# Optimization experiments

Measured on AMD Instinct MI355X. Metric: run time of the kernel, lower is better.

## Reference

```python
import jax, jax.numpy as jnp
import numpy as np

ALPHA = 1.0  # set_privacy(True)


def setup_inputs() -> dict:
    key = jax.random.key(0)
    k1, k2, k3, k4, k5, k6 = jax.random.split(key, 6)
    B, S, IN, OUT = 2, 1024, 4096, 11008
    NNZ = 2250000
    x = jax.random.normal(k1, (B, S, IN), dtype=jnp.float32)
    scales = jax.random.uniform(k2, (OUT,), dtype=jnp.float32)  # positive per-row scales
    ortho_vals = jax.random.normal(k3, (NNZ,), dtype=jnp.float32)
    base_packed = jax.random.randint(k4, (OUT, IN // 2), 0, 256, dtype=jnp.int32)
    ortho_rows = jnp.sort(jax.random.randint(k5, (NNZ,), 0, OUT, dtype=jnp.int32))
    ortho_cols = jax.random.randint(k6, (NNZ,), 0, IN, dtype=jnp.int32)
    return {"x": x, "scales": scales, "ortho_vals": ortho_vals,
            "base_packed": base_packed, "ortho_rows": ortho_rows, "ortho_cols": ortho_cols}


def _dequant_weight(base_packed, scales):
    OUT, HALF = base_packed.shape
    low = base_packed & 0xF          # packed column 2j  -> original column 2j
    high = (base_packed >> 4) & 0xF  # packed column 2j  -> original column 2j+1
    # interleave low/high nibbles back to [OUT, IN]
    w_off = jnp.stack([low, high], axis=-1).reshape(OUT, 2 * HALF)
    return (w_off.astype(jnp.float32) - 8.0) * scales[:, None]


def reference(x, scales, ortho_vals, base_packed, ortho_rows, ortho_cols):
    OUT = base_packed.shape[0]
    IN = base_packed.shape[1] * 2
    w_base = _dequant_weight(base_packed, scales)  # [OUT, IN] fp32
    w_sparse = jnp.zeros((OUT, IN), dtype=jnp.float32).at[ortho_rows, ortho_cols].add(
        ortho_vals.astype(jnp.float32))
    w = w_base + ALPHA * w_sparse
    x_flat = x.reshape(-1, IN).astype(jnp.float32)
    out = x_flat @ w.T  # [tokens, OUT]
    return out.reshape(x.shape[:-1] + (OUT,)).astype(x.dtype)
```

## Files before the change

### kernel.cpp

```cpp
#include <hip/hip_runtime.h>
#include <stdint.h>

#define ALPHA 1.0f

typedef int i32x4 __attribute__((ext_vector_type(4)));

typedef __attribute__((address_space(3))) void lds_void_t;
typedef const __attribute__((address_space(1))) void global_void_t;

__device__ __forceinline__ void async16(const void* g, void* l) {
    __builtin_amdgcn_global_load_lds((global_void_t*)g, (lds_void_t*)l, 16, 0, 0);
}

__device__ __forceinline__ signed char q8(float v, float inv) {
    float f = fminf(fmaxf(v * inv, -127.f), 127.f);
    return (signed char)__float2int_rn(f);
}

__global__ __launch_bounds__(256) void prep_kernel(
    const float* __restrict__ x, const int* __restrict__ rows,
    int* __restrict__ rstart, int* __restrict__ rend,
    signed char* __restrict__ X8, float* __restrict__ sx, int M, int nnz) {
    const int b = blockIdx.x;
    if (b < M) {
        __shared__ float red[4];
        const int t = threadIdx.x;
        const float4* xr = (const float4*)(x + (size_t)b * 4096);
        float4 v[4];
        float mx = 0.f;
#pragma unroll
        for (int i = 0; i < 4; i++) {
            v[i] = xr[t * 4 + i];
            mx = fmaxf(mx, fmaxf(fmaxf(fabsf(v[i].x), fabsf(v[i].y)),
                                 fmaxf(fabsf(v[i].z), fabsf(v[i].w))));
        }
#pragma unroll
        for (int o = 32; o > 0; o >>= 1) mx = fmaxf(mx, __shfl_xor(mx, o));
        if ((t & 63) == 0) red[t >> 6] = mx;
        __syncthreads();
        mx = fmaxf(fmaxf(red[0], red[1]), fmaxf(red[2], red[3]));
        mx = fmaxf(mx, 1e-20f);
        if (t == 0) sx[b] = mx / 127.f;
        const float inv = 127.f / mx;
        union { signed char c[16]; int4 w; } u;
#pragma unroll
        for (int i = 0; i < 4; i++) {
            u.c[i * 4 + 0] = q8(v[i].x, inv);
            u.c[i * 4 + 1] = q8(v[i].y, inv);
            u.c[i * 4 + 2] = q8(v[i].z, inv);
            u.c[i * 4 + 3] = q8(v[i].w, inv);
        }
        ((int4*)(X8 + (size_t)b * 4096))[t] = u.w;
    } else {
        int i = (b - M) * 256 + threadIdx.x;
        if (i < nnz) {
            int r = rows[i];
            if (i == 0 || rows[i - 1] != r) rstart[r] = i;
            if (i == nnz - 1 || rows[i + 1] != r) rend[r] = i + 1;
        }
    }
}

__global__ __launch_bounds__(256) void build_w8_kernel(
    const int* __restrict__ packed, const float* __restrict__ scales,
    const float* __restrict__ vals, const int* __restrict__ cols,
    const int* __restrict__ rstart, const int* __restrict__ rend,
    signed char* __restrict__ W8, float* __restrict__ sw) {
    __shared__ __align__(16) float acc[4096];
    __shared__ float red[4];
    const int r = blockIdx.x;
    const int t = threadIdx.x;
    const float s = scales[r];

    const int4* prow4 = (const int4*)(packed + (size_t)r * 2048);
    int4 p0 = prow4[2 * t], p1 = prow4[2 * t + 1];

    const int lo = rstart[r], hi = rend[r];

    float4 sp[4] = {float4{0,0,0,0}, float4{0,0,0,0},
                    float4{0,0,0,0}, float4{0,0,0,0}};
    if (hi > lo) {
        char* ab = (char*)acc;
#pragma unroll
        for (int i = 0; i < 4; i++) {
            int b = 64 * t + 16 * i;
            *(float4*)(ab + (b ^ (((b >> 7) & 7) << 4))) = float4{0, 0, 0, 0};
        }
        __syncthreads();
        for (int i = lo + t; i < hi; i += 256) {
            int b = cols[i] * 4;
            atomicAdd((float*)(ab + (b ^ (((b >> 7) & 7) << 4))),
                      vals[i] * ALPHA);
        }
        __syncthreads();
#pragma unroll
        for (int i = 0; i < 4; i++) {
            int b = 64 * t + 16 * i;
            sp[i] = *(const float4*)(ab + (b ^ (((b >> 7) & 7) << 4)));
        }
    }

    float w[16];
    {
        int pv[8] = {p0.x, p0.y, p0.z, p0.w, p1.x, p1.y, p1.z, p1.w};
#pragma unroll
        for (int q = 0; q < 8; q++) {
            w[2 * q]     = (float)((pv[q] & 0xF) - 8) * s;
            w[2 * q + 1] = (float)(((pv[q] >> 4) & 0xF) - 8) * s;
        }
    }
    const float* spf = (const float*)sp;
    float mx = 0.f;
#pragma unroll
    for (int k = 0; k < 16; k++) {
        w[k] += spf[k];
        mx = fmaxf(mx, fabsf(w[k]));
    }
#pragma unroll
    for (int o = 32; o > 0; o >>= 1) mx = fmaxf(mx, __shfl_xor(mx, o));
    if ((t & 63) == 0) red[t >> 6] = mx;
    __syncthreads();
    mx = fmaxf(fmaxf(red[0], red[1]), fmaxf(red[2], red[3]));
    mx = fmaxf(mx, 1e-20f);
    if (t == 0) sw[r] = mx / 127.f;
    const float inv = 127.f / mx;

    union { signed char c[16]; int4 v; } u;
#pragma unroll
    for (int k = 0; k < 16; k++) u.c[k] = q8(w[k], inv);
    ((int4*)(W8 + (size_t)r * 4096))[t] = u.v;
}

__global__ __launch_bounds__(512) void gemm_kernel(
    const signed char* __restrict__ Xq,
    const signed char* __restrict__ Wq,
    const float* __restrict__ sx,
    const float* __restrict__ sw,
    float* __restrict__ C,
    int M, int N, int K) {
    __shared__ __align__(16) signed char smem[3 * 49152];

    const int tid  = threadIdx.x;
    const int wid  = tid >> 6;
    const int lane = tid & 63;
    const int wr = wid >> 2;
    const int wc = wid & 3;

    const int nwg = gridDim.x;
    const int bid = blockIdx.x;
    const int qc = nwg >> 3, rr = nwg & 7;
    const int xcd = bid & 7, loc = bid >> 3;
    const int swz = (xcd < rr ? xcd * (qc + 1) : rr * (qc + 1) + (xcd - rr) * qc) + loc;
    const int tm = M >> 7;
    const int mt = swz % tm;
    const int nt = swz / tm;
    const int m0 = mt << 7;
    const int n0 = nt << 8;

    const int sr = tid >> 3;
    const int sc = ((tid & 7) ^ (sr & 7)) << 4;
    const int lw0 = wid << 10;
    const int lw1 = 8192 + (wid << 10);

    const signed char* Ax  = Xq + (size_t)m0 * K;
    const signed char* Bw0 = Wq + (size_t)n0 * K;
    const signed char* Bw1 = Wq + (size_t)(n0 + 128) * K;

#define STAGE(gbase, ldsbase) do {                                         \
        async16((gbase) + (size_t)sr * K + sc, (ldsbase) + lw0);           \
        async16((gbase) + (size_t)(sr + 64) * K + sc, (ldsbase) + lw1);    \
    } while (0)

    const int fm = lane & 15;
    const int slot0 = ((lane >> 4) ^ (lane & 7)) << 4;
    const int slot1 = slot0 ^ 64;
    const int arow_base = wr * 64;
    const int brow_base = wc * 64;

#define LDA(buf, mi, sl) \
    (*(const i32x4*)((buf) + (size_t)(arow_base + (mi) * 16 + fm) * 128 + (sl)))
#define LDB(buf, nj, sl) \
    (*(const i32x4*)((buf) + 16384 + (size_t)(brow_base + (nj) * 16 + fm) * 128 + (sl)))

#define MFMA8(m0i, m1i, aX, aY, B0, B1, B2, B3) do {                        \
        __builtin_amdgcn_s_setprio(1);                                      \
        acc[m0i][0] = __builtin_amdgcn_mfma_i32_16x16x64_i8(aX, B0, acc[m0i][0], 0, 0, 0); \
        acc[m1i][0] = __builtin_amdgcn_mfma_i32_16x16x64_i8(aY, B0, acc[m1i][0], 0, 0, 0); \
        acc[m0i][1] = __builtin_amdgcn_mfma_i32_16x16x64_i8(aX, B1, acc[m0i][1], 0, 0, 0); \
        acc[m1i][1] = __builtin_amdgcn_mfma_i32_16x16x64_i8(aY, B1, acc[m1i][1], 0, 0, 0); \
        acc[m0i][2] = __builtin_amdgcn_mfma_i32_16x16x64_i8(aX, B2, acc[m0i][2], 0, 0, 0); \
        acc[m1i][2] = __builtin_amdgcn_mfma_i32_16x16x64_i8(aY, B2, acc[m1i][2], 0, 0, 0); \
        acc[m0i][3] = __builtin_amdgcn_mfma_i32_16x16x64_i8(aX, B3, acc[m0i][3], 0, 0, 0); \
        acc[m1i][3] = __builtin_amdgcn_mfma_i32_16x16x64_i8(aY, B3, acc[m1i][3], 0, 0, 0); \
        __builtin_amdgcn_s_setprio(0);                                      \
    } while (0)

    i32x4 acc[4][4];
#pragma unroll
    for (int i = 0; i < 4; i++)
#pragma unroll
        for (int j = 0; j < 4; j++) acc[i][j] = (i32x4){0, 0, 0, 0};

    const int NT = K >> 7;

    STAGE(Ax,        smem);
    STAGE(Bw0,       smem + 16384);
    STAGE(Bw1,       smem + 32768);
    STAGE(Ax  + 128, smem + 49152);
    STAGE(Bw0 + 128, smem + 49152 + 16384);
    STAGE(Bw1 + 128, smem + 49152 + 32768);
    asm volatile("s_waitcnt vmcnt(6)" ::: "memory");
    __builtin_amdgcn_s_barrier();
    __builtin_amdgcn_sched_barrier(0);

    int cur = 0;
    for (int it = 0; it < NT; ++it) {
        signed char* Ab = smem + cur * 49152;
        int pb = cur + 2; if (pb >= 3) pb -= 3;
        signed char* PA = smem + pb * 49152;
        const bool pref = (it + 2 < NT);
        const int kc = (it + 2) << 7;

        i32x4 a0  = LDA(Ab, 0, slot0), a1  = LDA(Ab, 1, slot0);
        i32x4 bA0 = LDB(Ab, 0, slot0), bA1 = LDB(Ab, 1, slot0),
              bA2 = LDB(Ab, 2, slot0), bA3 = LDB(Ab, 3, slot0);
        i32x4 na0 = LDA(Ab, 2, slot0), na1 = LDA(Ab, 3, slot0);
        if (pref) STAGE(Ax + kc, PA);
        MFMA8(0, 1, a0, a1, bA0, bA1, bA2, bA3);

        i32x4 bB0 = LDB(Ab, 0, slot1), bB1 = LDB(Ab, 1, slot1),
              bB2 = LDB(Ab, 2, slot1), bB3 = LDB(Ab, 3, slot1);
        i32x4 ma0 = LDA(Ab, 0, slot1), ma1 = LDA(Ab, 1, slot1);
        if (pref) STAGE(Bw0 + kc, PA + 16384);
        MFMA8(2, 3, na0, na1, bA0, bA1, bA2, bA3);

        i32x4 pa2 = LDA(Ab, 2, slot1), pa3 = LDA(Ab, 3, slot1);
        if (pref) STAGE(Bw1 + kc, PA + 32768);
        MFMA8(0, 1, ma0, ma1, bB0, bB1, bB2, bB3);

        if (it + 2 < NT)       { asm volatile("s_waitcnt vmcnt(6)" ::: "memory"); }
        else if (it + 2 == NT) { asm volatile("s_waitcnt vmcnt(0)" ::: "memory"); }
        MFMA8(2, 3, pa2, pa3, bB0, bB1, bB2, bB3);

        __builtin_amdgcn_s_barrier();
        __builtin_amdgcn_sched_barrier(0);
        cur += 1; if (cur == 3) cur = 0;
    }
#undef STAGE
#undef LDA
#undef LDB
#undef MFMA8

    const int cr = (lane >> 4) << 2;
    const int cc = lane & 15;
#pragma unroll
    for (int mi = 0; mi < 4; ++mi) {
        const int row0 = m0 + wr * 64 + mi * 16 + cr;
        float sxv[4];
#pragma unroll
        for (int r = 0; r < 4; ++r) sxv[r] = sx[row0 + r];
#pragma unroll
        for (int nj = 0; nj < 4; ++nj) {
            const int col = n0 + wc * 64 + nj * 16 + cc;
            const float swc = sw[col];
            float* cp = C + (size_t)row0 * N + col;
#pragma unroll
            for (int r = 0; r < 4; ++r)
                cp[(size_t)r * N] = (float)acc[mi][nj][r] * sxv[r] * swc;
        }
    }
}

extern "C" void kernel_launch(void* const* d_in, const int* in_sizes, int n_in,
                              void* d_out, int out_size, void* d_ws, size_t ws_size,
                              hipStream_t stream) {
    const float* x      = (const float*)d_in[0];
    const float* scales = (const float*)d_in[1];
    const float* vals   = (const float*)d_in[2];
    const int* packed   = (const int*)d_in[3];
    const int* rows     = (const int*)d_in[4];
    const int* cols     = (const int*)d_in[5];
    float* out          = (float*)d_out;

    const int OUT  = in_sizes[1];
    const int HALF = in_sizes[3] / OUT;
    const int IN   = HALF * 2;
    const int M    = in_sizes[0] / IN;
    const int NNZ  = in_sizes[2];

    signed char* W8 = (signed char*)d_ws;
    signed char* X8 = W8 + (size_t)OUT * IN;
    float* sx   = (float*)(X8 + (size_t)M * IN);
    float* sw   = sx + M;
    int* rstart = (int*)(sw + OUT);
    int* rend   = rstart + OUT;

    const int boundsBlocks = (NNZ + 255) / 256;
    prep_kernel<<<M + boundsBlocks, 256, 0, stream>>>(x, rows, rstart, rend,
                                                      X8, sx, M, NNZ);
    build_w8_kernel<<<OUT, 256, 0, stream>>>(packed, scales, vals, cols,
                                             rstart, rend, W8, sw);
    const int nwg = (M / 128) * (OUT / 256);
    gemm_kernel<<<nwg, 512, 0, stream>>>(X8, W8, sx, sw, out, M, OUT, IN);
}
```

Before: 314.1 us.

## Load X operand directly from global to registers, stage only weights in LDS

Result: slower. 461.0 us (+46.8%).

```diff
diff --git a/kernel.cpp b/kernel.cpp
--- a/kernel.cpp
+++ b/kernel.cpp
@@ -138,7 +138,7 @@
     const float* __restrict__ sw,
     float* __restrict__ C,
     int M, int N, int K) {
-    __shared__ __align__(16) signed char smem[3 * 49152];
+    __shared__ __align__(16) signed char smem[3 * 32768];
 
     const int tid  = threadIdx.x;
     const int wid  = tid >> 6;
@@ -151,9 +151,9 @@
     const int qc = nwg >> 3, rr = nwg & 7;
     const int xcd = bid & 7, loc = bid >> 3;
     const int swz = (xcd < rr ? xcd * (qc + 1) : rr * (qc + 1) + (xcd - rr) * qc) + loc;
-    const int tm = M >> 7;
-    const int mt = swz % tm;
-    const int nt = swz / tm;
+    const int tn = N >> 8;
+    const int nt = swz % tn;
+    const int mt = swz / tn;
     const int m0 = mt << 7;
     const int n0 = nt << 8;
 
@@ -162,7 +162,6 @@
     const int lw0 = wid << 10;
     const int lw1 = 8192 + (wid << 10);
 
-    const signed char* Ax  = Xq + (size_t)m0 * K;
     const signed char* Bw0 = Wq + (size_t)n0 * K;
     const signed char* Bw1 = Wq + (size_t)(n0 + 128) * K;
 
@@ -172,15 +171,19 @@
     } while (0)
 
     const int fm = lane & 15;
+    const int fk16 = (lane >> 4) << 4;
     const int slot0 = ((lane >> 4) ^ (lane & 7)) << 4;
     const int slot1 = slot0 ^ 64;
     const int arow_base = wr * 64;
     const int brow_base = wc * 64;
 
-#define LDA(buf, mi, sl) \
-    (*(const i32x4*)((buf) + (size_t)(arow_base + (mi) * 16 + fm) * 128 + (sl)))
+    const signed char* Arow =
+        Xq + (size_t)(m0 + arow_base + fm) * K + fk16;
+
+#define LDAG(mi, ks, kb) \
+    (*(const i32x4*)(Arow + (size_t)(mi) * 16 * K + (kb) + (ks) * 64))
 #define LDB(buf, nj, sl) \
-    (*(const i32x4*)((buf) + 16384 + (size_t)(brow_base + (nj) * 16 + fm) * 128 + (sl)))
+    (*(const i32x4*)((buf) + (size_t)(brow_base + (nj) * 16 + fm) * 128 + (sl)))
 
 #define MFMA8(m0i, m1i, aX, aY, B0, B1, B2, B3) do {                        \
         __builtin_amdgcn_s_setprio(1);                                      \
@@ -203,43 +206,41 @@
 
     const int NT = K >> 7;
 
-    STAGE(Ax,        smem);
-    STAGE(Bw0,       smem + 16384);
-    STAGE(Bw1,       smem + 32768);
-    STAGE(Ax  + 128, smem + 49152);
-    STAGE(Bw0 + 128, smem + 49152 + 16384);
-    STAGE(Bw1 + 128, smem + 49152 + 32768);
-    asm volatile("s_waitcnt vmcnt(6)" ::: "memory");
+    STAGE(Bw0,       smem);
+    STAGE(Bw1,       smem + 16384);
+    STAGE(Bw0 + 128, smem + 32768);
+    STAGE(Bw1 + 128, smem + 32768 + 16384);
+    asm volatile("s_waitcnt vmcnt(4)" ::: "memory");
     __builtin_amdgcn_s_barrier();
     __builtin_amdgcn_sched_barrier(0);
 
     int cur = 0;
     for (int it = 0; it < NT; ++it) {
-        signed char* Ab = smem + cur * 49152;
+        signed char* Bb = smem + cur * 32768;
         int pb = cur + 2; if (pb >= 3) pb -= 3;
-        signed char* PA = smem + pb * 49152;
+        signed char* PB = smem + pb * 32768;
         const bool pref = (it + 2 < NT);
         const int kc = (it + 2) << 7;
-
-        i32x4 a0  = LDA(Ab, 0, slot0), a1  = LDA(Ab, 1, slot0);
-        i32x4 bA0 = LDB(Ab, 0, slot0), bA1 = LDB(Ab, 1, slot0),
-              bA2 = LDB(Ab, 2, slot0), bA3 = LDB(Ab, 3, slot0);
-        i32x4 na0 = LDA(Ab, 2, slot0), na1 = LDA(Ab, 3, slot0);
-        if (pref) STAGE(Ax + kc, PA);
+        const int k0 = it << 7;
+
+        i32x4 a0  = LDAG(0, 0, k0), a1  = LDAG(1, 0, k0);
+        i32x4 na0 = LDAG(2, 0, k0), na1 = LDAG(3, 0, k0);
+        i32x4 ma0 = LDAG(0, 1, k0), ma1 = LDAG(1, 1, k0);
+        i32x4 bA0 = LDB(Bb, 0, slot0), bA1 = LDB(Bb, 1, slot0),
+              bA2 = LDB(Bb, 2, slot0), bA3 = LDB(Bb, 3, slot0);
         MFMA8(0, 1, a0, a1, bA0, bA1, bA2, bA3);
 
-        i32x4 bB0 = LDB(Ab, 0, slot1), bB1 = LDB(Ab, 1, slot1),
-              bB2 = LDB(Ab, 2, slot1), bB3 = LDB(Ab, 3, slot1);
-        i32x4 ma0 = LDA(Ab, 0, slot1), ma1 = LDA(Ab, 1, slot1);
-        if (pref) STAGE(Bw0 + kc, PA + 16384);
+        i32x4 pa2 = LDAG(2, 1, k0), pa3 = LDAG(3, 1, k0);
+        i32x4 bB0 = LDB(Bb, 0, slot1), bB1 = LDB(Bb, 1, slot1),
+              bB2 = LDB(Bb, 2, slot1), bB3 = LDB(Bb, 3, slot1);
+        if (pref) STAGE(Bw0 + kc, PB);
         MFMA8(2, 3, na0, na1, bA0, bA1, bA2, bA3);
 
-        i32x4 pa2 = LDA(Ab, 2, slot1), pa3 = LDA(Ab, 3, slot1);
-        if (pref) STAGE(Bw1 + kc, PA + 32768);
+        if (pref) STAGE(Bw1 + kc, PB + 16384);
         MFMA8(0, 1, ma0, ma1, bB0, bB1, bB2, bB3);
 
-        if (it + 2 < NT)       { asm volatile("s_waitcnt vmcnt(6)" ::: "memory"); }
-        else if (it + 2 == NT) { asm volatile("s_waitcnt vmcnt(0)" ::: "memory"); }
+        if (it + 2 < NT)      { asm volatile("s_waitcnt vmcnt(12)" ::: "memory"); }
+        else if (it + 1 < NT) { asm volatile("s_waitcnt vmcnt(8)"  ::: "memory"); }
         MFMA8(2, 3, pa2, pa3, bB0, bB1, bB2, bB3);
 
         __builtin_amdgcn_s_barrier();
@@ -247,7 +248,7 @@
         cur += 1; if (cur == 3) cur = 0;
     }
 #undef STAGE
-#undef LDA
+#undef LDAG
 #undef LDB
 #undef MFMA8
 
```

## Use 4-wave GEMM blocks with 64x128 per-wave tiles

Applied to the files above, without the earlier changes.

Result: slower. 343.0 us (+9.2%).

```diff
diff --git a/kernel.cpp b/kernel.cpp
--- a/kernel.cpp
+++ b/kernel.cpp
@@ -131,7 +131,7 @@
     ((int4*)(W8 + (size_t)r * 4096))[t] = u.v;
 }
 
-__global__ __launch_bounds__(512) void gemm_kernel(
+__global__ __launch_bounds__(256, 1) void gemm_kernel(
     const signed char* __restrict__ Xq,
     const signed char* __restrict__ Wq,
     const float* __restrict__ sx,
@@ -143,8 +143,8 @@
     const int tid  = threadIdx.x;
     const int wid  = tid >> 6;
     const int lane = tid & 63;
-    const int wr = wid >> 2;
-    const int wc = wid & 3;
+    const int wr = wid >> 1;
+    const int wc = wid & 1;
 
     const int nwg = gridDim.x;
     const int bid = blockIdx.x;
@@ -159,57 +159,71 @@
 
     const int sr = tid >> 3;
     const int sc = ((tid & 7) ^ (sr & 7)) << 4;
-    const int lw0 = wid << 10;
-    const int lw1 = 8192 + (wid << 10);
-
-    const signed char* Ax  = Xq + (size_t)m0 * K;
-    const signed char* Bw0 = Wq + (size_t)n0 * K;
-    const signed char* Bw1 = Wq + (size_t)(n0 + 128) * K;
-
-#define STAGE(gbase, ldsbase) do {                                         \
-        async16((gbase) + (size_t)sr * K + sc, (ldsbase) + lw0);           \
-        async16((gbase) + (size_t)(sr + 64) * K + sc, (ldsbase) + lw1);    \
+    const int lw = wid << 10;
+
+    const signed char* Ax = Xq + (size_t)m0 * K;
+    const signed char* Bw = Wq + (size_t)n0 * K;
+
+#define STAGE_A(gbase, ldsbase) do {                                         \
+        _Pragma("unroll")                                                    \
+        for (int i_ = 0; i_ < 4; i_++)                                       \
+            async16((gbase) + (size_t)(i_ * 32 + sr) * K + sc,               \
+                    (ldsbase) + i_ * 4096 + lw);                             \
+    } while (0)
+#define STAGE_B(gbase, ldsbase, h) do {                                      \
+        _Pragma("unroll")                                                    \
+        for (int i_ = 0; i_ < 4; i_++)                                       \
+            async16((gbase) + (size_t)((h) * 128 + i_ * 32 + sr) * K + sc,   \
+                    (ldsbase) + 16384 + (h) * 16384 + i_ * 4096 + lw);       \
     } while (0)
 
     const int fm = lane & 15;
     const int slot0 = ((lane >> 4) ^ (lane & 7)) << 4;
     const int slot1 = slot0 ^ 64;
     const int arow_base = wr * 64;
-    const int brow_base = wc * 64;
+    const int brow_base = wc * 128;
 
 #define LDA(buf, mi, sl) \
     (*(const i32x4*)((buf) + (size_t)(arow_base + (mi) * 16 + fm) * 128 + (sl)))
 #define LDB(buf, nj, sl) \
     (*(const i32x4*)((buf) + 16384 + (size_t)(brow_base + (nj) * 16 + fm) * 128 + (sl)))
 
-#define MFMA8(m0i, m1i, aX, aY, B0, B1, B2, B3) do {                        \
+#define MFMA16(A0_, A1_, A2_, A3_, B0_, B1_, B2_, B3_, njb) do {            \
         __builtin_amdgcn_s_setprio(1);                                      \
-        acc[m0i][0] = __builtin_amdgcn_mfma_i32_16x16x64_i8(aX, B0, acc[m0i][0], 0, 0, 0); \
-        acc[m1i][0] = __builtin_amdgcn_mfma_i32_16x16x64_i8(aY, B0, acc[m1i][0], 0, 0, 0); \
-        acc[m0i][1] = __builtin_amdgcn_mfma_i32_16x16x64_i8(aX, B1, acc[m0i][1], 0, 0, 0); \
-        acc[m1i][1] = __builtin_amdgcn_mfma_i32_16x16x64_i8(aY, B1, acc[m1i][1], 0, 0, 0); \
-        acc[m0i][2] = __builtin_amdgcn_mfma_i32_16x16x64_i8(aX, B2, acc[m0i][2], 0, 0, 0); \
-        acc[m1i][2] = __builtin_amdgcn_mfma_i32_16x16x64_i8(aY, B2, acc[m1i][2], 0, 0, 0); \
-        acc[m0i][3] = __builtin_amdgcn_mfma_i32_16x16x64_i8(aX, B3, acc[m0i][3], 0, 0, 0); \
-        acc[m1i][3] = __builtin_amdgcn_mfma_i32_16x16x64_i8(aY, B3, acc[m1i][3], 0, 0, 0); \
+        acc[0][(njb)+0] = __builtin_amdgcn_mfma_i32_16x16x64_i8(A0_, B0_, acc[0][(njb)+0], 0, 0, 0); \
+        acc[1][(njb)+0] = __builtin_amdgcn_mfma_i32_16x16x64_i8(A1_, B0_, acc[1][(njb)+0], 0, 0, 0); \
+        acc[2][(njb)+0] = __builtin_amdgcn_mfma_i32_16x16x64_i8(A2_, B0_, acc[2][(njb)+0], 0, 0, 0); \
+        acc[3][(njb)+0] = __builtin_amdgcn_mfma_i32_16x16x64_i8(A3_, B0_, acc[3][(njb)+0], 0, 0, 0); \
+        acc[0][(njb)+1] = __builtin_amdgcn_mfma_i32_16x16x64_i8(A0_, B1_, acc[0][(njb)+1], 0, 0, 0); \
+        acc[1][(njb)+1] = __builtin_amdgcn_mfma_i32_16x16x64_i8(A1_, B1_, acc[1][(njb)+1], 0, 0, 0); \
+        acc[2][(njb)+1] = __builtin_amdgcn_mfma_i32_16x16x64_i8(A2_, B1_, acc[2][(njb)+1], 0, 0, 0); \
+        acc[3][(njb)+1] = __builtin_amdgcn_mfma_i32_16x16x64_i8(A3_, B1_, acc[3][(njb)+1], 0, 0, 0); \
+        acc[0][(njb)+2] = __builtin_amdgcn_mfma_i32_16x16x64_i8(A0_, B2_, acc[0][(njb)+2], 0, 0, 0); \
+        acc[1][(njb)+2] = __builtin_amdgcn_mfma_i32_16x16x64_i8(A1_, B2_, acc[1][(njb)+2], 0, 0, 0); \
+        acc[2][(njb)+2] = __builtin_amdgcn_mfma_i32_16x16x64_i8(A2_, B2_, acc[2][(njb)+2], 0, 0, 0); \
+        acc[3][(njb)+2] = __builtin_amdgcn_mfma_i32_16x16x64_i8(A3_, B2_, acc[3][(njb)+2], 0, 0, 0); \
+        acc[0][(njb)+3] = __builtin_amdgcn_mfma_i32_16x16x64_i8(A0_, B3_, acc[0][(njb)+3], 0, 0, 0); \
+        acc[1][(njb)+3] = __builtin_amdgcn_mfma_i32_16x16x64_i8(A1_, B3_, acc[1][(njb)+3], 0, 0, 0); \
+        acc[2][(njb)+3] = __builtin_amdgcn_mfma_i32_16x16x64_i8(A2_, B3_, acc[2][(njb)+3], 0, 0, 0); \
+        acc[3][(njb)+3] = __builtin_amdgcn_mfma_i32_16x16x64_i8(A3_, B3_, acc[3][(njb)+3], 0, 0, 0); \
         __builtin_amdgcn_s_setprio(0);                                      \
     } while (0)
 
-    i32x4 acc[4][4];
+    i32x4 acc[4][8];
 #pragma unroll
     for (int i = 0; i < 4; i++)
 #pragma unroll
-        for (int j = 0; j < 4; j++) acc[i][j] = (i32x4){0, 0, 0, 0};
+        for (int j = 0; j < 8; j++) acc[i][j] = (i32x4){0, 0, 0, 0};
 
     const int NT = K >> 7;
 
-    STAGE(Ax,        smem);
-    STAGE(Bw0,       smem + 16384);
-    STAGE(Bw1,       smem + 32768);
-    STAGE(Ax  + 128, smem + 49152);
-    STAGE(Bw0 + 128, smem + 49152 + 16384);
-    STAGE(Bw1 + 128, smem + 49152 + 32768);
-    asm volatile("s_waitcnt vmcnt(6)" ::: "memory");
+    STAGE_A(Ax,       smem);
+    STAGE_B(Bw,       smem, 0);
+    STAGE_B(Bw,       smem, 1);
+    STAGE_A(Ax + 128, smem + 49152);
+    STAGE_B(Bw + 128, smem + 49152, 0);
+    STAGE_B(Bw + 128, smem + 49152, 1);
+    asm volatile("s_waitcnt vmcnt(12)" ::: "memory");
     __builtin_amdgcn_s_barrier();
     __builtin_amdgcn_sched_barrier(0);
 
@@ -221,35 +235,40 @@
         const bool pref = (it + 2 < NT);
         const int kc = (it + 2) << 7;
 
-        i32x4 a0  = LDA(Ab, 0, slot0), a1  = LDA(Ab, 1, slot0);
-        i32x4 bA0 = LDB(Ab, 0, slot0), bA1 = LDB(Ab, 1, slot0),
-              bA2 = LDB(Ab, 2, slot0), bA3 = LDB(Ab, 3, slot0);
-        i32x4 na0 = LDA(Ab, 2, slot0), na1 = LDA(Ab, 3, slot0);
-        if (pref) STAGE(Ax + kc, PA);
-        MFMA8(0, 1, a0, a1, bA0, bA1, bA2, bA3);
-
-        i32x4 bB0 = LDB(Ab, 0, slot1), bB1 = LDB(Ab, 1, slot1),
-              bB2 = LDB(Ab, 2, slot1), bB3 = LDB(Ab, 3, slot1);
-        i32x4 ma0 = LDA(Ab, 0, slot1), ma1 = LDA(Ab, 1, slot1);
-        if (pref) STAGE(Bw0 + kc, PA + 16384);
-        MFMA8(2, 3, na0, na1, bA0, bA1, bA2, bA3);
-
-        i32x4 pa2 = LDA(Ab, 2, slot1), pa3 = LDA(Ab, 3, slot1);
-        if (pref) STAGE(Bw1 + kc, PA + 32768);
-        MFMA8(0, 1, ma0, ma1, bB0, bB1, bB2, bB3);
-
-        if (it + 2 < NT)       { asm volatile("s_waitcnt vmcnt(6)" ::: "memory"); }
-        else if (it + 2 == NT) { asm volatile("s_waitcnt vmcnt(0)" ::: "memory"); }
-        MFMA8(2, 3, pa2, pa3, bB0, bB1, bB2, bB3);
+        i32x4 aA0 = LDA(Ab, 0, slot0), aA1 = LDA(Ab, 1, slot0),
+              aA2 = LDA(Ab, 2, slot0), aA3 = LDA(Ab, 3, slot0);
+        i32x4 bL0 = LDB(Ab, 0, slot0), bL1 = LDB(Ab, 1, slot0),
+              bL2 = LDB(Ab, 2, slot0), bL3 = LDB(Ab, 3, slot0);
+        i32x4 bH0 = LDB(Ab, 4, slot0), bH1 = LDB(Ab, 5, slot0),
+              bH2 = LDB(Ab, 6, slot0), bH3 = LDB(Ab, 7, slot0);
+        if (pref) STAGE_A(Ax + kc, PA);
+        MFMA16(aA0, aA1, aA2, aA3, bL0, bL1, bL2, bL3, 0);
+
+        i32x4 aK0 = LDA(Ab, 0, slot1), aK1 = LDA(Ab, 1, slot1),
+              aK2 = LDA(Ab, 2, slot1), aK3 = LDA(Ab, 3, slot1);
+        i32x4 cL0 = LDB(Ab, 0, slot1), cL1 = LDB(Ab, 1, slot1),
+              cL2 = LDB(Ab, 2, slot1), cL3 = LDB(Ab, 3, slot1);
+        if (pref) STAGE_B(Bw + kc, PA, 0);
+        MFMA16(aA0, aA1, aA2, aA3, bH0, bH1, bH2, bH3, 4);
+
+        i32x4 cH0 = LDB(Ab, 4, slot1), cH1 = LDB(Ab, 5, slot1),
+              cH2 = LDB(Ab, 6, slot1), cH3 = LDB(Ab, 7, slot1);
+        if (pref) STAGE_B(Bw + kc, PA, 1);
+        MFMA16(aK0, aK1, aK2, aK3, cL0, cL1, cL2, cL3, 0);
+
+        if (it + 2 < NT)       { asm volatile("s_waitcnt vmcnt(12)" ::: "memory"); }
+        else if (it + 2 == NT) { asm volatile("s_waitcnt vmcnt(0)"  ::: "memory"); }
+        MFMA16(aK0, aK1, aK2, aK3, cH0, cH1, cH2, cH3, 4);
 
         __builtin_amdgcn_s_barrier();
         __builtin_amdgcn_sched_barrier(0);
         cur += 1; if (cur == 3) cur = 0;
     }
-#undef STAGE
+#undef STAGE_A
+#undef STAGE_B
 #undef LDA
 #undef LDB
-#undef MFMA8
+#undef MFMA16
 
     const int cr = (lane >> 4) << 2;
     const int cc = lane & 15;
@@ -260,8 +279,8 @@
 #pragma unroll
         for (int r = 0; r < 4; ++r) sxv[r] = sx[row0 + r];
 #pragma unroll
-        for (int nj = 0; nj < 4; ++nj) {
-            const int col = n0 + wc * 64 + nj * 16 + cc;
+        for (int nj = 0; nj < 8; ++nj) {
+            const int col = n0 + wc * 128 + nj * 16 + cc;
             const float swc = sw[col];
             float* cp = C + (size_t)row0 * N + col;
 #pragma unroll
@@ -301,5 +320,5 @@
     build_w8_kernel<<<OUT, 256, 0, stream>>>(packed, scales, vals, cols,
                                              rstart, rend, W8, sw);
     const int nwg = (M / 128) * (OUT / 256);
-    gemm_kernel<<<nwg, 512, 0, stream>>>(X8, W8, sx, sw, out, M, OUT, IN);
-}
+    gemm_kernel<<<nwg, 256, 0, stream>>>(X8, W8, sx, sw, out, M, OUT, IN);
+}
```
